# Kernel optimization log

Measured on AMD Instinct MI355X. Metric: run time of the kernel, lower is better.

The kernel has to match this reference:

```python
import jax, jax.numpy as jnp
import numpy as np

B, S, D, H = 4, 1024, 512, 8
DH = D // H  # dim_head = 64
LN_EPS = 1e-5
COS_EPS = 1e-8


def setup_inputs() -> dict:
    key = jax.random.key(0)
    ks = jax.random.split(key, 8)
    q = jax.random.normal(ks[0], (B, S, D), dtype=jnp.float32)
    k = jax.random.normal(ks[1], (B, S, D), dtype=jnp.float32)
    v = jax.random.normal(ks[2], (B, S, D), dtype=jnp.float32)
    ln_g = jnp.ones((D,), jnp.float32)
    ln_b = jnp.zeros((D,), jnp.float32)
    W_in = jax.random.normal(ks[3], (D, D), dtype=jnp.float32) / np.sqrt(D)
    W_out = jax.random.normal(ks[4], (D, D), dtype=jnp.float32) / np.sqrt(D)
    b_out = jnp.zeros((D,), jnp.float32)
    cov_w = jnp.float32(0.6)
    var_w = jnp.float32(0.2)
    return {"q": q, "k": k, "v": v, "ln_g": ln_g, "ln_b": ln_b,
            "W_in": W_in, "W_out": W_out, "b_out": b_out,
            "cov_w": cov_w, "var_w": var_w}


def reference(q, k, v, ln_g, ln_b, W_in, W_out, b_out, cov_w, var_w):
    def transform(x):
        # input_layernorm followed by bias-free input_linear
        mu = jnp.mean(x, axis=-1, keepdims=True)
        var = jnp.var(x, axis=-1, keepdims=True)
        xn = (x - mu) * jax.lax.rsqrt(var + LN_EPS) * ln_g + ln_b
        y = xn @ W_in
        # 'q n (h d) -> h q n d'
        return y.reshape(B, S, H, DH).transpose(2, 0, 1, 3)

    f_q = transform(q)  # [h, b, n, d]
    f_k = transform(k)  # [h, b, m, d]
    f_v = transform(v)  # [h, b, m, d]

    # cosine_distance(f_q, f_k^T)
    dots = jnp.einsum('hbnd,hbmd->hbnm', f_q, f_k)
    qn = jnp.linalg.norm(f_q, axis=-1)  # [h, b, n]
    kn = jnp.linalg.norm(f_k, axis=-1)  # [h, b, m]
    cosine_sim = dots / (qn[..., :, None] * kn[..., None, :] + COS_EPS)

    # basic_attention_components
    q_c = f_q - jnp.mean(f_q, axis=-1, keepdims=True)
    k_c = f_k - jnp.mean(f_k, axis=-1, keepdims=True)
    cov_component = jnp.einsum('hbnd,hbmd->hbnm', q_c, k_c) / DH
    q_var = jnp.var(f_q, axis=-1, ddof=1)  # torch.var unbiased=True
    k_var = jnp.var(f_k, axis=-1, ddof=1)
    var_component = (q_var[..., :, None] * k_var[..., None, :]) / DH

    # fixed learned-scalar mixing (dynamic_weight=False path)
    attn = (cov_w * cov_component + var_w * var_component
            + (1.0 - cov_w - var_w) * cosine_sim)

    out = jnp.einsum('hbnm,hbmd->hbnd', attn, f_v)
    # 'h q n d -> q n (h d)'
    out = out.transpose(1, 2, 0, 3).reshape(B, S, D)
    return out @ W_out + b_out
```

## Files before the change

kernel.cpp:

```cpp
#include <hip/hip_runtime.h>


#define R_TOT 4096
#define DD 512
#define HB_N 32

typedef __attribute__((ext_vector_type(8))) short short8;
typedef __attribute__((ext_vector_type(4))) float f32x4;

static __device__ inline unsigned short f2bf(float f) {
    union { float f; unsigned u; } x{f};
    unsigned r = x.u + 0x7fff + ((x.u >> 16) & 1);
    return (unsigned short)(r >> 16);
}

static __device__ inline unsigned scale2(unsigned u, float a, float b) {
    float lo = __uint_as_float(u << 16);
    float hi = __uint_as_float(u & 0xffff0000u);
    return (unsigned)f2bf(lo * a) | ((unsigned)f2bf(hi * b) << 16);
}

__global__ __launch_bounds__(256) void k1_ln_prep(
    const float* __restrict__ q, const float* __restrict__ k, const float* __restrict__ v,
    const float* __restrict__ ln_g, const float* __restrict__ ln_b,
    const float* __restrict__ Win, const float* __restrict__ Wout,
    unsigned short* __restrict__ xn, unsigned short* __restrict__ WinT,
    unsigned short* __restrict__ WoutT)
{
    int blk = blockIdx.x;
    int t = threadIdx.x;
    if (blk < 3 * R_TOT) {
        const float* src = (blk < R_TOT) ? q : (blk < 2 * R_TOT ? k : v);
        const float* x = src + (size_t)(blk & (R_TOT - 1)) * DD;
        float2 val = *(const float2*)(x + t * 2);
        float s = val.x + val.y;
        float s2 = val.x * val.x + val.y * val.y;
        #pragma unroll
        for (int o = 32; o; o >>= 1) { s += __shfl_xor(s, o); s2 += __shfl_xor(s2, o); }
        __shared__ float red[8];
        int wv = t >> 6;
        if ((t & 63) == 0) { red[wv] = s; red[4 + wv] = s2; }
        __syncthreads();
        s = red[0] + red[1] + red[2] + red[3];
        s2 = red[4] + red[5] + red[6] + red[7];
        float mu = s * (1.f / 512.f);
        float var = s2 * (1.f / 512.f) - mu * mu;
        float rstd = rsqrtf(var + 1e-5f);
        float2 gg = *(const float2*)(ln_g + t * 2);
        float2 bb = *(const float2*)(ln_b + t * 2);
        unsigned short* o = xn + (size_t)blk * DD + t * 2;
        o[0] = f2bf((val.x - mu) * rstd * gg.x + bb.x);
        o[1] = f2bf((val.y - mu) * rstd * gg.y + bb.y);
    } else {
        __shared__ float tl[64][65];
        int bb = blk - 3 * R_TOT;
        const float* src = (bb & 64) ? Wout : Win;
        unsigned short* dst = (bb & 64) ? WoutT : WinT;
        int tile = bb & 63;
        int r0 = (tile >> 3) * 64, c0 = (tile & 7) * 64;
        #pragma unroll
        for (int rep = 0; rep < 16; rep++) {
            int rr = rep * 4 + (t >> 6), cc = t & 63;
            tl[rr][cc] = src[(size_t)(r0 + rr) * DD + c0 + cc];
        }
        __syncthreads();
        #pragma unroll
        for (int rep = 0; rep < 16; rep++) {
            int rr = rep * 4 + (t >> 6), cc = t & 63;
            dst[(size_t)(c0 + rr) * DD + r0 + cc] = f2bf(tl[cc][rr]);
        }
    }
}

__global__ __launch_bounds__(256) void gemm_qkv(
    const unsigned short* __restrict__ A, const unsigned short* __restrict__ Bt,
    unsigned short* __restrict__ A2, unsigned short* __restrict__ Lt,
    unsigned short* __restrict__ Vt)
{
    __shared__ __align__(16) char smbuf[39936];
    unsigned short (*As)[40] = (unsigned short(*)[40])smbuf;
    unsigned short (*Bs)[40] = (unsigned short(*)[40])(smbuf + 10240);
    int t = threadIdx.x, lane = t & 63, wv = t >> 6;
    int quad = lane >> 4, l15 = lane & 15;
    int m0 = blockIdx.y * 128, n0 = blockIdx.x * 128;
    int wr = (wv >> 1) * 64, wc = (wv & 1) * 64;
    f32x4 acc[4][4] = {};
    for (int kt = 0; kt < 512; kt += 32) {
        __syncthreads();
        #pragma unroll
        for (int ld = 0; ld < 2; ld++) {
            int id = ld * 256 + t;
            int row = id >> 2, co = (id & 3) * 8;
            *(uint4*)&As[row][co] = *(const uint4*)(A + (size_t)(m0 + row) * 512 + kt + co);
            *(uint4*)&Bs[row][co] = *(const uint4*)(Bt + (size_t)(n0 + row) * 512 + kt + co);
        }
        __syncthreads();
        short8 af[4], bf[4];
        #pragma unroll
        for (int i = 0; i < 4; i++) af[i] = *(const short8*)&As[wr + i * 16 + l15][quad * 8];
        #pragma unroll
        for (int j = 0; j < 4; j++) bf[j] = *(const short8*)&Bs[wc + j * 16 + l15][quad * 8];
        #pragma unroll
        for (int i = 0; i < 4; i++)
            #pragma unroll
            for (int j = 0; j < 4; j++)
                acc[i][j] = __builtin_amdgcn_mfma_f32_16x16x32_bf16(af[i], bf[j], acc[i][j], 0, 0, 0);
    }
    __syncthreads();

    unsigned short* tile = (unsigned short*)(smbuf + wv * 9216);
    float* st     = (float*)(smbuf + 36864 + wv * 768);
    float* st_inv = st;
    float* st_var = st + 64;
    float* st_mu  = st + 128;

    int typ  = m0 >> 12;
    int rloc = (m0 & 4095) + wr;
    int b = rloc >> 10, sb = rloc & 1023;
    int h = (n0 + wc) >> 6;
    int hb = h * 4 + b;

    if (typ < 2) {
        #pragma unroll
        for (int i = 0; i < 4; i++)
            #pragma unroll
            for (int r = 0; r < 4; r++) {
                float a0 = acc[i][0][r], a1 = acc[i][1][r], a2 = acc[i][2][r], a3 = acc[i][3][r];
                float s1 = a0 + a1 + a2 + a3;
                float s2 = a0 * a0 + a1 * a1 + a2 * a2 + a3 * a3;
                #pragma unroll
                for (int o = 1; o < 16; o <<= 1) { s1 += __shfl_xor(s1, o); s2 += __shfl_xor(s2, o); }
                if (l15 == 0) {
                    int sl = i * 16 + quad * 4 + r;
                    float mu = s1 * (1.f / 64.f);
                    st_inv[sl] = rsqrtf(fmaxf(s2, 1e-20f));
                    st_var[sl] = (s2 - 64.f * mu * mu) * (1.f / 63.f);
                    st_mu[sl]  = mu;
                }
            }
    }
    #pragma unroll
    for (int i = 0; i < 4; i++)
        #pragma unroll
        for (int j = 0; j < 4; j++)
            #pragma unroll
            for (int r = 0; r < 4; r++) {
                int sl = i * 16 + quad * 4 + r, d = j * 16 + l15;
                unsigned short bv = f2bf(acc[i][j][r]);
                tile[(typ == 0) ? (sl * 72 + d) : (d * 72 + sl)] = bv;
            }

    if (typ == 0) {
        unsigned short* ob = A2 + ((size_t)hb * 1024 + sb) * 160;
        #pragma unroll
        for (int it = 0; it < 8; it++) {
            int sl = it * 8 + (lane >> 3), ch = (lane & 7) * 8;
            uint4 raw = *(uint4*)&tile[sl * 72 + ch];
            *(uint4*)(ob + (size_t)sl * 160 + ch) = raw;
            float iv = st_inv[sl];
            uint4 o2;
            o2.x = scale2(raw.x, iv, iv); o2.y = scale2(raw.y, iv, iv);
            o2.z = scale2(raw.z, iv, iv); o2.w = scale2(raw.w, iv, iv);
            *(uint4*)(ob + (size_t)sl * 160 + 64 + ch) = o2;
        }
        {
            int sl = lane;
            uint4 z = {0, 0, 0, 0};
            uint4 t0 = z;
            t0.x = (unsigned)f2bf(st_var[sl]) | ((unsigned)f2bf(st_mu[sl]) << 16);
            unsigned short* p = ob + (size_t)sl * 160 + 128;
            *(uint4*)p = t0;
            *(uint4*)(p + 8) = z; *(uint4*)(p + 16) = z; *(uint4*)(p + 24) = z;
        }
    } else if (typ == 1) {
        unsigned short* lb = Lt + (size_t)hb * 160 * 1024 + sb;
        #pragma unroll
        for (int it = 0; it < 8; it++) {
            int d = it * 8 + (lane >> 3), ch = (lane & 7) * 8;
            uint4 raw = *(uint4*)&tile[d * 72 + ch];
            *(uint4*)(lb + (size_t)d * 1024 + ch) = raw;
            const float* ivp = st_inv + ch;
            uint4 o2;
            o2.x = scale2(raw.x, ivp[0], ivp[1]); o2.y = scale2(raw.y, ivp[2], ivp[3]);
            o2.z = scale2(raw.z, ivp[4], ivp[5]); o2.w = scale2(raw.w, ivp[6], ivp[7]);
            *(uint4*)(lb + (size_t)(64 + d) * 1024 + ch) = o2;
        }
        if (lane < 16) {
            int which = lane >> 3, ch = (lane & 7) * 8;
            const float* sp = (which ? st_mu : st_var) + ch;
            uint4 o;
            o.x = (unsigned)f2bf(sp[0]) | ((unsigned)f2bf(sp[1]) << 16);
            o.y = (unsigned)f2bf(sp[2]) | ((unsigned)f2bf(sp[3]) << 16);
            o.z = (unsigned)f2bf(sp[4]) | ((unsigned)f2bf(sp[5]) << 16);
            o.w = (unsigned)f2bf(sp[6]) | ((unsigned)f2bf(sp[7]) << 16);
            *(uint4*)(lb + (size_t)(128 + which) * 1024 + ch) = o;
        }
        uint4 z = {0, 0, 0, 0};
        for (int zi = lane; zi < 240; zi += 64) {
            int d = 130 + (zi >> 3), ch = (zi & 7) * 8;
            *(uint4*)(lb + (size_t)d * 1024 + ch) = z;
        }
    } else {
        unsigned short* vb = Vt + (size_t)hb * 64 * 1024 + sb;
        #pragma unroll
        for (int it = 0; it < 8; it++) {
            int d = it * 8 + (lane >> 3), ch = (lane & 7) * 8;
            uint4 raw = *(uint4*)&tile[d * 72 + ch];
            *(uint4*)(vb + (size_t)d * 1024 + ch) = raw;
        }
    }
}

__global__ __launch_bounds__(256) void gemm512(
    const unsigned short* __restrict__ A, const unsigned short* __restrict__ Bt,
    float* __restrict__ C, const float* __restrict__ bias)
{
    __shared__ __align__(16) unsigned short As[128][40];
    __shared__ __align__(16) unsigned short Bs[128][40];
    int t = threadIdx.x, lane = t & 63, wv = t >> 6;
    int quad = lane >> 4, l15 = lane & 15;
    int m0 = blockIdx.y * 128, n0 = blockIdx.x * 128;
    int wr = (wv >> 1) * 64, wc = (wv & 1) * 64;
    f32x4 acc[4][4] = {};
    for (int kt = 0; kt < 512; kt += 32) {
        __syncthreads();
        #pragma unroll
        for (int ld = 0; ld < 2; ld++) {
            int id = ld * 256 + t;
            int row = id >> 2, co = (id & 3) * 8;
            *(uint4*)&As[row][co] = *(const uint4*)(A + (size_t)(m0 + row) * 512 + kt + co);
            *(uint4*)&Bs[row][co] = *(const uint4*)(Bt + (size_t)(n0 + row) * 512 + kt + co);
        }
        __syncthreads();
        short8 af[4], bf[4];
        #pragma unroll
        for (int i = 0; i < 4; i++) af[i] = *(const short8*)&As[wr + i * 16 + l15][quad * 8];
        #pragma unroll
        for (int j = 0; j < 4; j++) bf[j] = *(const short8*)&Bs[wc + j * 16 + l15][quad * 8];
        #pragma unroll
        for (int i = 0; i < 4; i++)
            #pragma unroll
            for (int j = 0; j < 4; j++)
                acc[i][j] = __builtin_amdgcn_mfma_f32_16x16x32_bf16(af[i], bf[j], acc[i][j], 0, 0, 0);
    }
    #pragma unroll
    for (int i = 0; i < 4; i++)
        #pragma unroll
        for (int j = 0; j < 4; j++)
            #pragma unroll
            for (int r = 0; r < 4; r++) {
                int rr = m0 + wr + i * 16 + quad * 4 + r;
                int cc = n0 + wc + j * 16 + l15;
                float vv = acc[i][j][r];
                if (bias) vv += bias[cc];
                C[(size_t)rr * 512 + cc] = vv;
            }
}

__global__ __launch_bounds__(256) void k4_ktv(
    const unsigned short* __restrict__ Lt, const unsigned short* __restrict__ Vt,
    float* __restrict__ Cpart)
{
    int hb = blockIdx.x, kt = blockIdx.y;
    int t = threadIdx.x, lane = t & 63, wv = t >> 6;
    int quad = lane >> 4, l15 = lane & 15;
    __shared__ __align__(16) unsigned short As[160][72];
    __shared__ __align__(16) unsigned short Bs[64][72];
    const unsigned short* Ab = Lt + (size_t)hb * 160 * 1024 + kt * 128;
    const unsigned short* Bb = Vt + (size_t)hb * 64 * 1024 + kt * 128;
    f32x4 acc[10] = {};
    for (int kc = 0; kc < 128; kc += 64) {
        __syncthreads();
        #pragma unroll
        for (int i = 0; i < 5; i++) {
            int id = i * 256 + t;
            int row = id >> 3, co = (id & 7) * 8;
            *(uint4*)&As[row][co] = *(const uint4*)(Ab + (size_t)row * 1024 + kc + co);
        }
        #pragma unroll
        for (int i = 0; i < 2; i++) {
            int id = i * 256 + t;
            int row = id >> 3, co = (id & 7) * 8;
            *(uint4*)&Bs[row][co] = *(const uint4*)(Bb + (size_t)row * 1024 + kc + co);
        }
        __syncthreads();
        #pragma unroll
        for (int kk = 0; kk < 2; kk++) {
            short8 bfrag = *(const short8*)&Bs[wv * 16 + l15][kk * 32 + quad * 8];
            #pragma unroll
            for (int mt = 0; mt < 10; mt++) {
                short8 afrag = *(const short8*)&As[mt * 16 + l15][kk * 32 + quad * 8];
                acc[mt] = __builtin_amdgcn_mfma_f32_16x16x32_bf16(afrag, bfrag, acc[mt], 0, 0, 0);
            }
        }
    }
    float* ob = Cpart + ((size_t)hb * 8 + kt) * (160 * 64);
    #pragma unroll
    for (int mt = 0; mt < 10; mt++)
        #pragma unroll
        for (int r = 0; r < 4; r++)
            ob[(mt * 16 + quad * 4 + r) * 64 + wv * 16 + l15] = acc[mt][r];
}

__global__ __launch_bounds__(256) void k5_reduce(
    const float* __restrict__ Cpart, unsigned short* __restrict__ B2t,
    const float* __restrict__ covp, const float* __restrict__ varp)
{
    int hb = blockIdx.x, t = threadIdx.x;
    float cov = covp[0], vw = varp[0];
    float c1 = cov * (1.f / 64.f), cw = 1.f - cov - vw;
    float vw64 = vw * (1.f / 64.f), c2 = -cov;
    const float* base = Cpart + (size_t)hb * 8 * 10240;
    unsigned short* ob = B2t + (size_t)hb * 10240;
    #pragma unroll 4
    for (int rep = 0; rep < 32; rep++) {
        int o = rep * 256 + t;
        int kk = o >> 6, d = o & 63;
        float s = 0;
        #pragma unroll
        for (int c = 0; c < 8; c++) s += base[c * 10240 + kk * 64 + d];
        ob[d * 160 + kk] = f2bf((kk < 64) ? c1 * s : cw * s);
    }
    if (t < 128) {
        int d = t & 63, which = t >> 6;
        int off = 8192 + which * 64 + d;
        float s = 0;
        #pragma unroll
        for (int c = 0; c < 8; c++) s += base[c * 10240 + off];
        ob[d * 160 + 128 + which] = f2bf(which ? c2 * s : vw64 * s);
    }
    for (int o = t; o < 64 * 30; o += 256) {
        int d = o / 30, kk = 130 + o % 30;
        ob[d * 160 + kk] = 0;
    }
}

__global__ __launch_bounds__(256) void k6_apply(
    const unsigned short* __restrict__ A2, const unsigned short* __restrict__ B2t,
    unsigned short* __restrict__ g)
{
    int hb = blockIdx.y, h = hb >> 2, b = hb & 3;
    int m0 = blockIdx.x * 128;
    int t = threadIdx.x, lane = t & 63, wv = t >> 6;
    int quad = lane >> 4, l15 = lane & 15;
    __shared__ __align__(16) unsigned short As[128][40];
    __shared__ __align__(16) unsigned short Bs[64][40];
    const unsigned short* Ab = A2 + (size_t)hb * 1024 * 160;
    const unsigned short* Bb = B2t + (size_t)hb * 10240;
    f32x4 acc[2][4] = {};
    for (int kt = 0; kt < 160; kt += 32) {
        __syncthreads();
        #pragma unroll
        for (int ld = 0; ld < 2; ld++) {
            int id = ld * 256 + t;
            int row = id >> 2, co = (id & 3) * 8;
            *(uint4*)&As[row][co] = *(const uint4*)(Ab + (size_t)(m0 + row) * 160 + kt + co);
        }
        {
            int row = t >> 2, co = (t & 3) * 8;
            *(uint4*)&Bs[row][co] = *(const uint4*)(Bb + (size_t)row * 160 + kt + co);
        }
        __syncthreads();
        short8 af[2], bf[4];
        #pragma unroll
        for (int i = 0; i < 2; i++) af[i] = *(const short8*)&As[wv * 32 + i * 16 + l15][quad * 8];
        #pragma unroll
        for (int j = 0; j < 4; j++) bf[j] = *(const short8*)&Bs[j * 16 + l15][quad * 8];
        #pragma unroll
        for (int i = 0; i < 2; i++)
            #pragma unroll
            for (int j = 0; j < 4; j++)
                acc[i][j] = __builtin_amdgcn_mfma_f32_16x16x32_bf16(af[i], bf[j], acc[i][j], 0, 0, 0);
    }
    #pragma unroll
    for (int i = 0; i < 2; i++)
        #pragma unroll
        for (int j = 0; j < 4; j++)
            #pragma unroll
            for (int r = 0; r < 4; r++) {
                int rr = m0 + wv * 32 + i * 16 + quad * 4 + r;
                int cc = j * 16 + l15;
                g[((size_t)b * 1024 + rr) * 512 + h * 64 + cc] = f2bf(acc[i][j][r]);
            }
}

extern "C" void kernel_launch(void* const* d_in, const int* in_sizes, int n_in,
                              void* d_out, int out_size, void* d_ws, size_t ws_size,
                              hipStream_t stream)
{
    const float* q    = (const float*)d_in[0];
    const float* k    = (const float*)d_in[1];
    const float* v    = (const float*)d_in[2];
    const float* ln_g = (const float*)d_in[3];
    const float* ln_b = (const float*)d_in[4];
    const float* Win  = (const float*)d_in[5];
    const float* Wout = (const float*)d_in[6];
    const float* bout = (const float*)d_in[7];
    const float* covw = (const float*)d_in[8];
    const float* varw = (const float*)d_in[9];

    char* ws = (char*)d_ws;
    size_t off = 0;
    auto alloc = [&](size_t bytes) { size_t r = off; off += (bytes + 255) & ~(size_t)255; return r; };
    unsigned short* xn    = (unsigned short*)(ws + alloc((size_t)3 * R_TOT * DD * 2));
    unsigned short* WinT  = (unsigned short*)(ws + alloc((size_t)DD * DD * 2));
    unsigned short* WoutT = (unsigned short*)(ws + alloc((size_t)DD * DD * 2));
    unsigned short* A2    = (unsigned short*)(ws + alloc((size_t)HB_N * 1024 * 160 * 2));
    unsigned short* Lt    = (unsigned short*)(ws + alloc((size_t)HB_N * 160 * 1024 * 2));
    unsigned short* Vt    = (unsigned short*)(ws + alloc((size_t)HB_N * 64 * 1024 * 2));
    float*          Cpart = (float*)(ws + alloc((size_t)HB_N * 8 * 10240 * 4));
    unsigned short* g     = (unsigned short*)(ws + alloc((size_t)R_TOT * DD * 2));
    unsigned short* B2t   = (unsigned short*)(ws + alloc((size_t)HB_N * 10240 * 2));
    (void)ws_size; (void)in_sizes; (void)n_in; (void)out_size;

    k1_ln_prep<<<3 * R_TOT + 128, 256, 0, stream>>>(q, k, v, ln_g, ln_b, Win, Wout, xn, WinT, WoutT);
    gemm_qkv<<<dim3(4, 96), 256, 0, stream>>>(xn, WinT, A2, Lt, Vt);
    k4_ktv<<<dim3(HB_N, 8), 256, 0, stream>>>(Lt, Vt, Cpart);
    k5_reduce<<<HB_N, 256, 0, stream>>>(Cpart, B2t, covw, varw);
    k6_apply<<<dim3(8, HB_N), 256, 0, stream>>>(A2, B2t, g);
    gemm512<<<dim3(4, 32), 256, 0, stream>>>(g, WoutT, (float*)d_out, bout);
}
```

Baseline: 162.7 us.

## Use direct global-to-LDS loads with XOR swizzle in QKV GEMM; parallelize reduce

The QKV projection GEMM now fills shared memory with global_load_lds direct copies instead of register round-trips. It also doubles the K-step to 64 and uses an XOR-swizzled LDS layout so fragment reads avoid bank conflicts. The reduce kernel is split across 5 column-chunk blocks per head-batch, with the per-column scaling and zero padding folded into one expression. The aim is less load latency and fewer barriers in the main GEMM, plus more parallelism in the small reduction. The risk is that the GEMM keeps a synchronous barrier with no double buffering, so the async loads may not overlap compute much.

```diff
diff --git a/kernel.cpp b/kernel.cpp
--- a/kernel.cpp
+++ b/kernel.cpp
@@ -18,6 +18,12 @@
     float lo = __uint_as_float(u << 16);
     float hi = __uint_as_float(u & 0xffff0000u);
     return (unsigned)f2bf(lo * a) | ((unsigned)f2bf(hi * b) << 16);
+}
+
+static __device__ inline void async_cp16(const unsigned short* g, unsigned short* l) {
+    __builtin_amdgcn_global_load_lds(
+        (const __attribute__((address_space(1))) unsigned int*)g,
+        (__attribute__((address_space(3))) unsigned int*)l, 16, 0, 0);
 }
 
 __global__ __launch_bounds__(256) void k1_ln_prep(
@@ -78,33 +84,40 @@
     unsigned short* __restrict__ Vt)
 {
     __shared__ __align__(16) char smbuf[39936];
-    unsigned short (*As)[40] = (unsigned short(*)[40])smbuf;
-    unsigned short (*Bs)[40] = (unsigned short(*)[40])(smbuf + 10240);
+    unsigned short* AsF = (unsigned short*)smbuf;
+    unsigned short* BsF = (unsigned short*)(smbuf + 16384);
     int t = threadIdx.x, lane = t & 63, wv = t >> 6;
     int quad = lane >> 4, l15 = lane & 15;
     int m0 = blockIdx.y * 128, n0 = blockIdx.x * 128;
     int wr = (wv >> 1) * 64, wc = (wv & 1) * 64;
+    int swz = l15 & 7;
+    int r8 = lane >> 3, cc8 = lane & 7;
     f32x4 acc[4][4] = {};
-    for (int kt = 0; kt < 512; kt += 32) {
-        __syncthreads();
-        #pragma unroll
-        for (int ld = 0; ld < 2; ld++) {
-            int id = ld * 256 + t;
-            int row = id >> 2, co = (id & 3) * 8;
-            *(uint4*)&As[row][co] = *(const uint4*)(A + (size_t)(m0 + row) * 512 + kt + co);
-            *(uint4*)&Bs[row][co] = *(const uint4*)(Bt + (size_t)(n0 + row) * 512 + kt + co);
-        }
-        __syncthreads();
-        short8 af[4], bf[4];
-        #pragma unroll
-        for (int i = 0; i < 4; i++) af[i] = *(const short8*)&As[wr + i * 16 + l15][quad * 8];
-        #pragma unroll
-        for (int j = 0; j < 4; j++) bf[j] = *(const short8*)&Bs[wc + j * 16 + l15][quad * 8];
-        #pragma unroll
-        for (int i = 0; i < 4; i++)
-            #pragma unroll
-            for (int j = 0; j < 4; j++)
-                acc[i][j] = __builtin_amdgcn_mfma_f32_16x16x32_bf16(af[i], bf[j], acc[i][j], 0, 0, 0);
+    for (int kt = 0; kt < 512; kt += 64) {
+        __syncthreads();
+        #pragma unroll
+        for (int gi = 0; gi < 4; gi++) {
+            int grp = wv * 4 + gi;
+            int row = grp * 8 + r8;
+            int col = kt + ((cc8 ^ (row & 7)) << 3);
+            async_cp16(A + (size_t)(m0 + row) * 512 + col, AsF + grp * 512);
+            async_cp16(Bt + (size_t)(n0 + row) * 512 + col, BsF + grp * 512);
+        }
+        __syncthreads();
+        #pragma unroll
+        for (int kk = 0; kk < 2; kk++) {
+            short8 af[4], bf[4];
+            int ksl = ((kk * 4 + quad) ^ swz) << 3;
+            #pragma unroll
+            for (int i = 0; i < 4; i++) af[i] = *(const short8*)&AsF[(wr + i * 16 + l15) * 64 + ksl];
+            #pragma unroll
+            for (int j = 0; j < 4; j++) bf[j] = *(const short8*)&BsF[(wc + j * 16 + l15) * 64 + ksl];
+            #pragma unroll
+            for (int i = 0; i < 4; i++)
+                #pragma unroll
+                for (int j = 0; j < 4; j++)
+                    acc[i][j] = __builtin_amdgcn_mfma_f32_16x16x32_bf16(af[i], bf[j], acc[i][j], 0, 0, 0);
+        }
     }
     __syncthreads();
 
@@ -306,32 +319,21 @@
     const float* __restrict__ Cpart, unsigned short* __restrict__ B2t,
     const float* __restrict__ covp, const float* __restrict__ varp)
 {
-    int hb = blockIdx.x, t = threadIdx.x;
+    int hb = blockIdx.x, c0 = blockIdx.y * 32, t = threadIdx.x;
     float cov = covp[0], vw = varp[0];
     float c1 = cov * (1.f / 64.f), cw = 1.f - cov - vw;
     float vw64 = vw * (1.f / 64.f), c2 = -cov;
     const float* base = Cpart + (size_t)hb * 8 * 10240;
     unsigned short* ob = B2t + (size_t)hb * 10240;
-    #pragma unroll 4
-    for (int rep = 0; rep < 32; rep++) {
+    #pragma unroll
+    for (int rep = 0; rep < 8; rep++) {
         int o = rep * 256 + t;
-        int kk = o >> 6, d = o & 63;
+        int kk = c0 + (o >> 6), d = o & 63;
         float s = 0;
         #pragma unroll
         for (int c = 0; c < 8; c++) s += base[c * 10240 + kk * 64 + d];
-        ob[d * 160 + kk] = f2bf((kk < 64) ? c1 * s : cw * s);
-    }
-    if (t < 128) {
-        int d = t & 63, which = t >> 6;
-        int off = 8192 + which * 64 + d;
-        float s = 0;
-        #pragma unroll
-        for (int c = 0; c < 8; c++) s += base[c * 10240 + off];
-        ob[d * 160 + 128 + which] = f2bf(which ? c2 * s : vw64 * s);
-    }
-    for (int o = t; o < 64 * 30; o += 256) {
-        int d = o / 30, kk = 130 + o % 30;
-        ob[d * 160 + kk] = 0;
+        float scale = (kk < 64) ? c1 : (kk < 128) ? cw : (kk == 128) ? vw64 : (kk == 129) ? c2 : 0.f;
+        ob[d * 160 + kk] = f2bf(scale * s);
     }
 }
 
@@ -416,7 +418,7 @@
     k1_ln_prep<<<3 * R_TOT + 128, 256, 0, stream>>>(q, k, v, ln_g, ln_b, Win, Wout, xn, WinT, WoutT);
     gemm_qkv<<<dim3(4, 96), 256, 0, stream>>>(xn, WinT, A2, Lt, Vt);
     k4_ktv<<<dim3(HB_N, 8), 256, 0, stream>>>(Lt, Vt, Cpart);
-    k5_reduce<<<HB_N, 256, 0, stream>>>(Cpart, B2t, covw, varw);
+    k5_reduce<<<dim3(HB_N, 5), 256, 0, stream>>>(Cpart, B2t, covw, varw);
     k6_apply<<<dim3(8, HB_N), 256, 0, stream>>>(A2, B2t, g);
     gemm512<<<dim3(4, 32), 256, 0, stream>>>(g, WoutT, (float*)d_out, bout);
 }
```

After: 153.7 us. 5.5% less time.
